# Kernel optimization log

Measured on AMD Instinct MI355X. Metric: run time of the kernel, lower is better.

## Reference

```python
import jax, jax.numpy as jnp
import numpy as np
import math

HIDDEN = 1024
HEADS = 16

def setup_inputs() -> dict:
    key = jax.random.key(0)
    k1, k2, k3 = jax.random.split(key, 3)
    B, T, C = 4, 2048, HIDDEN
    x = jax.random.normal(k1, (B, T, C), dtype=jnp.float32)
    w_qkv = jax.random.normal(k2, (C, 3 * C), dtype=jnp.float32) * (1.0 / math.sqrt(C))
    b_qkv = jnp.zeros((3 * C,), dtype=jnp.float32)
    w_out = jax.random.normal(k3, (C, C), dtype=jnp.float32) * (1.0 / math.sqrt(C))
    b_out = jnp.zeros((C,), dtype=jnp.float32)
    return {"x": x, "w_qkv": w_qkv, "b_qkv": b_qkv, "w_out": w_out, "b_out": b_out}

def reference(x, w_qkv, b_qkv, w_out, b_out):
    B, T, C = x.shape
    H = HEADS
    D = C // H  # head dim
    qkv = x @ w_qkv + b_qkv  # [B,T,3C]
    q, k, v = jnp.split(qkv, 3, axis=2)
    # [B,T,C] -> [B,H,T,D]
    q = q.reshape(B, T, H, D).transpose(0, 2, 1, 3)
    k = k.reshape(B, T, H, D).transpose(0, 2, 1, 3)
    v = v.reshape(B, T, H, D).transpose(0, 2, 1, 3)
    scale = 1.0 / math.sqrt(D)
    logits = jnp.einsum('bhqd,bhkd->bhqk', q, k) * scale  # [B,H,T,T]
    causal = jnp.tril(jnp.ones((T, T), dtype=bool))
    logits = jnp.where(causal[None, None, :, :], logits, -jnp.inf)
    probs = jax.nn.softmax(logits, axis=-1)
    out = jnp.einsum('bhqk,bhkd->bhqd', probs, v)  # [B,H,T,D]
    out = out.transpose(0, 2, 1, 3).reshape(B, T, C)
    return out @ w_out + b_out
```

## Files before the change

### kernel.cpp

```cpp
#include <hip/hip_runtime.h>
#include <hip/hip_bf16.h>

#define C_DIM  1024
#define NHEAD  16
#define DHEAD  64
#define T_LEN  2048
#define B_SZ   4
#define M_ROWS (B_SZ * T_LEN)
#define QKV_N  (3 * C_DIM)

typedef __bf16 bf16x8 __attribute__((ext_vector_type(8)));
typedef float  f32x4  __attribute__((ext_vector_type(4)));
typedef unsigned short ushort8_t __attribute__((ext_vector_type(8)));
typedef unsigned int   uint4_t   __attribute__((ext_vector_type(4)));
typedef short          short4_t  __attribute__((ext_vector_type(4)));

#if __has_builtin(__builtin_amdgcn_mfma_f32_16x16x16bf16_1k)
#define HAVE_MFMA_X16 1
#else
#define HAVE_MFMA_X16 0
#endif

__device__ __forceinline__ unsigned short f2bf(float f) {
    union { float f; unsigned int u; } v; v.f = f;
    unsigned int r = v.u + 0x7FFFu + ((v.u >> 16) & 1u);
    return (unsigned short)(r >> 16);
}

__device__ __forceinline__ bf16x8 as_bf16x8(ushort8_t u) {
    return __builtin_bit_cast(bf16x8, u);
}

__device__ __forceinline__ f32x4 mfma16(bf16x8 a, bf16x8 b, f32x4 c) {
    return __builtin_amdgcn_mfma_f32_16x16x32_bf16(a, b, c, 0, 0, 0);
}

#define GLL16(gsrc, ldst) __builtin_amdgcn_global_load_lds( \
    (const __attribute__((address_space(1))) void*)(gsrc),  \
    (__attribute__((address_space(3))) void*)(ldst), 16, 0, 0)

__device__ __forceinline__ int xcd_remap(int id, int nwg) {
    const int q = nwg >> 3, r = nwg & 7;
    const int xcd = id & 7, off = id >> 3;
    return (xcd < r) ? (xcd * (q + 1) + off) : (r * (q + 1) + (xcd - r) * q + off);
}

__global__ void k_convert(const float* __restrict__ in, unsigned short* __restrict__ out, int n4) {
    int i = blockIdx.x * blockDim.x + threadIdx.x;
    if (i >= n4) return;
    const float4 v = ((const float4*)in)[i];
    unsigned int lo = (unsigned int)f2bf(v.x) | ((unsigned int)f2bf(v.y) << 16);
    unsigned int hi = (unsigned int)f2bf(v.z) | ((unsigned int)f2bf(v.w) << 16);
    ((uint2*)out)[i] = make_uint2(lo, hi);
}

__global__ void k_transpose_bf16(const float* __restrict__ w, unsigned short* __restrict__ wT,
                                 int K, int N) {
    __shared__ float tile[32][33];
    const int n0 = blockIdx.x * 32, k0 = blockIdx.y * 32;
    const int tx = threadIdx.x, ty = threadIdx.y;
    for (int i = 0; i < 32; i += 8)
        tile[ty + i][tx] = w[(size_t)(k0 + ty + i) * N + (n0 + tx)];
    __syncthreads();
    for (int i = 0; i < 32; i += 8)
        wT[(size_t)(n0 + ty + i) * K + (k0 + tx)] = f2bf(tile[tx][ty + i]);
}

__global__ void k_transpose_v(const unsigned short* __restrict__ qkv,
                              unsigned short* __restrict__ vtg) {
    __shared__ unsigned short tile[32][33];
    const int tt = blockIdx.x;
    const int dy = blockIdx.y;
    const int bh = dy >> 1, dtile = dy & 1;
    const int b = bh >> 4, h = bh & 15;
    const int t0 = tt * 32, d0 = dtile * 32;
    const int tx = threadIdx.x, ty = threadIdx.y;
    const unsigned short* src = qkv + (size_t)b * T_LEN * QKV_N + 2 * C_DIM + h * DHEAD + d0;
    for (int i = 0; i < 32; i += 8)
        tile[ty + i][tx] = src[(size_t)(t0 + ty + i) * QKV_N + tx];
    __syncthreads();
    unsigned short* dst = vtg + ((size_t)bh * DHEAD + d0) * T_LEN + t0;
    for (int i = 0; i < 32; i += 8)
        dst[(size_t)(ty + i) * T_LEN + tx] = tile[tx][ty + i];
}

template<int BF16_OUT>
__global__ __launch_bounds__(256) void k_gemm(const unsigned short* __restrict__ A,
                       const unsigned short* __restrict__ Bt,
                       const float* __restrict__ bias,
                       void* __restrict__ C,
                       unsigned short* __restrict__ vtg,
                       int M, int N, int K) {
    __shared__ unsigned short As[128][64];
    __shared__ unsigned short Bs[128][64];

    const int tid  = threadIdx.x;
    const int lane = tid & 63;
    const int wv   = tid >> 6;
    const int wm = wv >> 1, wn = wv & 1;

    const int nwg = gridDim.x * gridDim.y;
    const int wg  = xcd_remap(blockIdx.y * gridDim.x + blockIdx.x, nwg);
    const int bx = wg % gridDim.x, by = wg / gridDim.x;
    const int m0 = by * 128;
    const int n0 = bx * 128;
    const int lr = lane & 15, lg = lane >> 4;

    f32x4 acc[4][4];
#pragma unroll
    for (int i = 0; i < 4; i++)
#pragma unroll
        for (int j = 0; j < 4; j++) acc[i][j] = (f32x4){0.f, 0.f, 0.f, 0.f};

    const int gr = lane >> 3;
    const int gc = 8 * ((lane & 7) ^ gr);

    for (int kt = 0; kt < K; kt += 64) {
        __syncthreads();
#pragma unroll
        for (int j = 0; j < 4; j++) {
            const int row = 32 * wv + 8 * j;
            GLL16(A  + (size_t)(m0 + row + gr) * K + kt + gc, &As[row][0]);
            GLL16(Bt + (size_t)(n0 + row + gr) * K + kt + gc, &Bs[row][0]);
        }
        __syncthreads();

#pragma unroll
        for (int s = 0; s < 2; s++) {
            const int cb = (s * 64 + lg * 16) ^ ((lr & 7) << 4);
            bf16x8 af[4], bfr[4];
#pragma unroll
            for (int i = 0; i < 4; i++)
                af[i] = as_bf16x8(*(const ushort8_t*)((const char*)&As[wm * 64 + i * 16 + lr][0] + cb));
#pragma unroll
            for (int j = 0; j < 4; j++)
                bfr[j] = as_bf16x8(*(const ushort8_t*)((const char*)&Bs[wn * 64 + j * 16 + lr][0] + cb));
#pragma unroll
            for (int i = 0; i < 4; i++)
#pragma unroll
                for (int j = 0; j < 4; j++)
                    acc[i][j] = mfma16(af[i], bfr[j], acc[i][j]);
        }
    }

    const bool isV = (vtg != nullptr) && (n0 >= 2 * C_DIM);
#pragma unroll
    for (int i = 0; i < 4; i++) {
#pragma unroll
        for (int j = 0; j < 4; j++) {
            const int col = n0 + wn * 64 + j * 16 + lr;
            const float bv = bias ? bias[col] : 0.f;
            if (isV) {
                const int dcol = col - 2 * C_DIM;
                const int hh = dcol >> 6, dd = dcol & 63;
                const int row0 = m0 + wm * 64 + i * 16 + lg * 4;
                const int bb = row0 >> 11, t0 = row0 & (T_LEN - 1);
                const unsigned int p0 = (unsigned int)f2bf(acc[i][j][0] + bv)
                                      | ((unsigned int)f2bf(acc[i][j][1] + bv) << 16);
                const unsigned int p1 = (unsigned int)f2bf(acc[i][j][2] + bv)
                                      | ((unsigned int)f2bf(acc[i][j][3] + bv) << 16);
                *(uint2*)&vtg[(((size_t)(bb * 16 + hh)) * 64 + dd) * T_LEN + t0] = make_uint2(p0, p1);
            } else {
#pragma unroll
                for (int r = 0; r < 4; r++) {
                    const int row = m0 + wm * 64 + i * 16 + lg * 4 + r;
                    const float v = acc[i][j][r] + bv;
                    if (BF16_OUT)
                        ((unsigned short*)C)[(size_t)row * N + col] = f2bf(v);
                    else
                        ((float*)C)[(size_t)row * N + col] = v;
                }
            }
        }
    }
}

#define KS_OFF(B_, ROW_) (((B_) << 13) + ((ROW_) << 7))
#define VS_OFF(B_, ROW_) (16384 + ((B_) << 13) + ((ROW_) << 7))
#define SCALE2 0.180336880f
__global__ __launch_bounds__(256, 2) void k_attn(const unsigned short* __restrict__ qkv,
                                                 const unsigned short* __restrict__ vtg,
                                                 unsigned short* __restrict__ out) {
    __shared__ __align__(16) char smem[32768];

    const int blk = xcd_remap(blockIdx.x, B_SZ * NHEAD * 16);
    const int pr = blk & 15;
    const int h  = (blk >> 4) & 15;
    const int b  = blk >> 8;
    const int bh = b * 16 + h;

    const int tid  = threadIdx.x;
    const int lane = tid & 63;
    const int w    = tid >> 6;
    const int lr = lane & 15, lg = lane >> 4;
    const int gr = lane >> 3;
    const int gc = 8 * ((lane & 7) ^ gr);
    const int ra = w * 16;

    const size_t base = (size_t)b * T_LEN * QKV_N + (size_t)h * DHEAD;
    const unsigned short* Qp = qkv + base;
    const unsigned short* Kp = qkv + base + C_DIM;
    const unsigned short* Vt = vtg + (size_t)bh * DHEAD * T_LEN;

    int buf = 0;
    for (int t = 0; t < 2; t++) {
        const int qt = (t == 0) ? pr : (31 - pr);
        const int qw = qt * 64 + w * 16;
        const int qg = qw + lr;
        const int R  = qt + 1;

        bf16x8 qf[2];
#pragma unroll
        for (int s = 0; s < 2; s++)
            qf[s] = as_bf16x8(*(const ushort8_t*)&Qp[(size_t)(qw + lr) * QKV_N + s * 32 + lg * 8]);

        f32x4 o[4];
#pragma unroll
        for (int f = 0; f < 4; f++) o[f] = (f32x4){0.f, 0.f, 0.f, 0.f};
        float lp = 0.f;

        GLL16(Kp + (size_t)(ra + gr) * QKV_N + gc,          smem + KS_OFF(buf, ra));
        GLL16(Kp + (size_t)(ra + 8 + gr) * QKV_N + gc,      smem + KS_OFF(buf, ra + 8));
        GLL16(Vt + (size_t)(ra + gr) * T_LEN + gc,          smem + VS_OFF(buf, ra));
        GLL16(Vt + (size_t)(ra + 8 + gr) * T_LEN + gc,      smem + VS_OFF(buf, ra + 8));

        for (int r = 0; r < R; ++r) {
            const int kb = r * 64;

            asm volatile("s_waitcnt vmcnt(0)" ::: "memory");
            __builtin_amdgcn_s_barrier();
            __builtin_amdgcn_sched_barrier(0);

            if (r + 1 < R) {
                const int kn = kb + 64;
                GLL16(Kp + (size_t)(kn + ra + gr) * QKV_N + gc,     smem + KS_OFF(buf ^ 1, ra));
                GLL16(Kp + (size_t)(kn + ra + 8 + gr) * QKV_N + gc, smem + KS_OFF(buf ^ 1, ra + 8));
                GLL16(Vt + (size_t)(ra + gr) * T_LEN + kn + gc,     smem + VS_OFF(buf ^ 1, ra));
                GLL16(Vt + (size_t)(ra + 8 + gr) * T_LEN + kn + gc, smem + VS_OFF(buf ^ 1, ra + 8));
            }

            f32x4 s4[4];
            __builtin_amdgcn_s_setprio(1);
#pragma unroll
            for (int f = 0; f < 4; f++) {
                const int row = f * 16 + lr;
                const bf16x8 kf0 = as_bf16x8(*(const ushort8_t*)
                    (smem + KS_OFF(buf, row) + ((lg * 16) ^ ((lr & 7) << 4))));
                const bf16x8 kf1 = as_bf16x8(*(const ushort8_t*)
                    (smem + KS_OFF(buf, row) + ((64 + lg * 16) ^ ((lr & 7) << 4))));
                f32x4 s = (f32x4){0.f, 0.f, 0.f, 0.f};
                s = mfma16(kf0, qf[0], s);
                s = mfma16(kf1, qf[1], s);
                s4[f] = s;
            }
            __builtin_amdgcn_s_setprio(0);

            const bool last = (r == R - 1);
            unsigned int pb[4][2];
#pragma unroll
            for (int f = 0; f < 4; f++) {
                unsigned short hh[4];
#pragma unroll
                for (int rr = 0; rr < 4; rr++) {
                    float sv = fminf(s4[f][rr] * SCALE2, 72.f);
                    if (last) {
                        const int kg = kb + f * 16 + lg * 4 + rr;
                        if (kg > qg) sv = -1e30f;
                    }
                    const float e = __builtin_amdgcn_exp2f(sv);
                    lp += e;
                    hh[rr] = __builtin_bit_cast(unsigned short, (__bf16)e);
                }
                pb[f][0] = (unsigned int)hh[0] | ((unsigned int)hh[1] << 16);
                pb[f][1] = (unsigned int)hh[2] | ((unsigned int)hh[3] << 16);
            }

            __builtin_amdgcn_s_setprio(1);
#pragma unroll
            for (int kg = 0; kg < 4; kg++) {
#if HAVE_MFMA_X16
                const short4_t pbv = __builtin_bit_cast(short4_t,
                    make_uint2(pb[kg][0], pb[kg][1]));
#else
                uint4_t pw;
                pw.x = pb[kg][0]; pw.y = pb[kg][1]; pw.z = 0u; pw.w = 0u;
                const bf16x8 pbv8 = __builtin_bit_cast(bf16x8, pw);
#endif
#pragma unroll
                for (int fd = 0; fd < 4; fd++) {
                    const int drow = fd * 16 + lr;
                    const uint2 va = *(const uint2*)(smem + VS_OFF(buf, drow) +
                                     ((kg * 32 + lg * 8) ^ ((lr & 7) << 4)));
#if HAVE_MFMA_X16
                    o[fd] = __builtin_amdgcn_mfma_f32_16x16x16bf16_1k(
                        __builtin_bit_cast(short4_t, va), pbv, o[fd], 0, 0, 0);
#else
                    uint4_t vw;
                    vw.x = va.x; vw.y = va.y; vw.z = va.x; vw.w = va.y;
                    o[fd] = mfma16(__builtin_bit_cast(bf16x8, vw), pbv8, o[fd]);
#endif
                }
            }
            __builtin_amdgcn_s_setprio(0);

            buf ^= 1;
        }

        lp += __shfl_xor(lp, 16, 64);
        lp += __shfl_xor(lp, 32, 64);
        const float inv = 1.f / lp;

#pragma unroll
        for (int fd = 0; fd < 4; fd++)
#pragma unroll
            for (int rr = 0; rr < 4; rr++) {
                const int d = fd * 16 + lg * 4 + rr;
                out[((size_t)b * T_LEN + qw + lr) * C_DIM + h * DHEAD + d] =
                    f2bf(o[fd][rr] * inv);
            }
    }
}

extern "C" void kernel_launch(void* const* d_in, const int* in_sizes, int n_in,
                              void* d_out, int out_size, void* d_ws, size_t ws_size,
                              hipStream_t stream) {
    const float* x      = (const float*)d_in[0];
    const float* w_qkv  = (const float*)d_in[1];
    const float* b_qkv  = (const float*)d_in[2];
    const float* w_out  = (const float*)d_in[3];
    const float* b_out  = (const float*)d_in[4];
    float* out = (float*)d_out;

    char* ws = (char*)d_ws;
    unsigned short* xb    = (unsigned short*)(ws);
    unsigned short* wqkvT = (unsigned short*)(ws + 16777216);
    unsigned short* woutT = (unsigned short*)(ws + 16777216 + 6291456);
    unsigned short* qkv   = (unsigned short*)(ws + 25165824);
    unsigned short* attn  = (unsigned short*)(ws + 75497472);

    const size_t VTG_OFF = 92274688ull;
    const bool fused_vt = (ws_size >= VTG_OFF + 16777216ull);
    unsigned short* vtg = fused_vt ? (unsigned short*)(ws + VTG_OFF)
                                   : (unsigned short*)(ws);

    {
        const int n4 = M_ROWS * C_DIM / 4;
        k_convert<<<(n4 + 255) / 256, 256, 0, stream>>>(x, xb, n4);
    }
    k_transpose_bf16<<<dim3(QKV_N / 32, C_DIM / 32), dim3(32, 8), 0, stream>>>(w_qkv, wqkvT, C_DIM, QKV_N);
    k_transpose_bf16<<<dim3(C_DIM / 32, C_DIM / 32), dim3(32, 8), 0, stream>>>(w_out, woutT, C_DIM, C_DIM);
    k_gemm<1><<<dim3(QKV_N / 128, M_ROWS / 128), 256, 0, stream>>>(
        xb, wqkvT, b_qkv, qkv, fused_vt ? vtg : nullptr, M_ROWS, QKV_N, C_DIM);
    if (!fused_vt)
        k_transpose_v<<<dim3(T_LEN / 32, 64 * 2), dim3(32, 8), 0, stream>>>(qkv, vtg);
    k_attn<<<B_SZ * NHEAD * 16, 256, 0, stream>>>(qkv, vtg, attn);
    k_gemm<0><<<dim3(C_DIM / 128, M_ROWS / 128), 256, 0, stream>>>(
        attn, woutT, b_out, out, nullptr, M_ROWS, C_DIM, C_DIM);
}
```

Baseline: 169.5 us.

## Use a 256x256-tile, 512-thread GEMM kernel for the QKV projection

Adds a new GEMM kernel for the QKV projection. It uses 256x256 output tiles, 8 waves and 128 KB of double-buffered dynamic LDS. The global-to-LDS loads for the next K tile are split into halves and interleaved with four MFMA phases separated by barriers. The fused V-transpose epilogue moves into the new kernel, and the old 128x128 kernel keeps only the plain output path for the output projection. Larger tiles raise operand reuse but give only 384 workgroups, so occupancy and wave balance may suffer, and the large LDS request may limit residency.

```diff
diff --git a/kernel.cpp b/kernel.cpp
--- a/kernel.cpp
+++ b/kernel.cpp
@@ -29,6 +29,10 @@
 
 __device__ __forceinline__ bf16x8 as_bf16x8(ushort8_t u) {
     return __builtin_bit_cast(bf16x8, u);
+}
+
+__device__ __forceinline__ bf16x8 ldsb(const char* p) {
+    return as_bf16x8(*(const ushort8_t*)p);
 }
 
 __device__ __forceinline__ f32x4 mfma16(bf16x8 a, bf16x8 b, f32x4 c) {
@@ -84,12 +88,191 @@
         dst[(size_t)(ty + i) * T_LEN + tx] = tile[tx][ty + i];
 }
 
+#define AS2(B_, R_) ((B_) * 32768 + (R_) * 128)
+#define BS2(B_, R_) (65536 + (B_) * 32768 + (R_) * 128)
+template<int BF16_OUT>
+__global__ __launch_bounds__(512, 2) void k_gemm256(const unsigned short* __restrict__ A,
+                       const unsigned short* __restrict__ Bt,
+                       const float* __restrict__ bias,
+                       void* __restrict__ C,
+                       unsigned short* __restrict__ vtg,
+                       int M, int N, int K) {
+    extern __shared__ char smem[];
+
+    const int tid  = threadIdx.x;
+    const int lane = tid & 63;
+    const int wv   = tid >> 6;
+    const int wm = wv >> 2, wn = wv & 3;
+    const int lr = lane & 15, lg = lane >> 4;
+    const int gr8 = lane >> 3;
+    const int gc  = 8 * ((lane & 7) ^ gr8);
+
+    const int gx  = gridDim.x;
+    const int nwg = gx * gridDim.y;
+    const int wg  = xcd_remap(blockIdx.y * gx + blockIdx.x, nwg);
+    const int bx = wg % gx, by = wg / gx;
+    const int m0 = by * 256, n0 = bx * 256;
+
+    f32x4 acc[8][4];
+#pragma unroll
+    for (int mi = 0; mi < 8; mi++)
+#pragma unroll
+        for (int ni = 0; ni < 4; ni++) acc[mi][ni] = (f32x4){0.f, 0.f, 0.f, 0.f};
+
+    {
+        const int R0 = wv * 16, R1 = 128 + wv * 16;
+        GLL16(A  + (size_t)(m0 + R0 + gr8) * K + gc,     smem + AS2(0, R0));
+        GLL16(A  + (size_t)(m0 + R0 + 8 + gr8) * K + gc, smem + AS2(0, R0 + 8));
+        GLL16(Bt + (size_t)(n0 + R0 + gr8) * K + gc,     smem + BS2(0, R0));
+        GLL16(Bt + (size_t)(n0 + R0 + 8 + gr8) * K + gc, smem + BS2(0, R0 + 8));
+        GLL16(A  + (size_t)(m0 + R1 + gr8) * K + gc,     smem + AS2(0, R1));
+        GLL16(A  + (size_t)(m0 + R1 + 8 + gr8) * K + gc, smem + AS2(0, R1 + 8));
+        GLL16(Bt + (size_t)(n0 + R1 + gr8) * K + gc,     smem + BS2(0, R1));
+        GLL16(Bt + (size_t)(n0 + R1 + 8 + gr8) * K + gc, smem + BS2(0, R1 + 8));
+    }
+
+    const int cb0 = (lg * 16) ^ ((lr & 7) << 4);
+    const int cb1 = (64 + lg * 16) ^ ((lr & 7) << 4);
+
+    int buf = 0;
+    for (int kt = 0; kt < K; kt += 64) {
+        const bool hn = (kt + 64 < K);
+        const int ktn = kt + 64;
+        const int bufn = buf ^ 1;
+
+        asm volatile("s_waitcnt vmcnt(0)" ::: "memory");
+        __builtin_amdgcn_s_barrier();
+        __builtin_amdgcn_sched_barrier(0);
+
+        bf16x8 af[4][2], bfv[2][2];
+
+        if (hn) {
+            const int R0 = wv * 16;
+            GLL16(A  + (size_t)(m0 + R0 + gr8) * K + ktn + gc,     smem + AS2(bufn, R0));
+            GLL16(A  + (size_t)(m0 + R0 + 8 + gr8) * K + ktn + gc, smem + AS2(bufn, R0 + 8));
+            GLL16(Bt + (size_t)(n0 + R0 + gr8) * K + ktn + gc,     smem + BS2(bufn, R0));
+            GLL16(Bt + (size_t)(n0 + R0 + 8 + gr8) * K + ktn + gc, smem + BS2(bufn, R0 + 8));
+        }
+#pragma unroll
+        for (int mi = 0; mi < 4; mi++) {
+            const char* p = smem + AS2(buf, wm * 128 + mi * 16 + lr);
+            af[mi][0] = ldsb(p + cb0); af[mi][1] = ldsb(p + cb1);
+        }
+#pragma unroll
+        for (int ni = 0; ni < 2; ni++) {
+            const char* p = smem + BS2(buf, wn * 64 + ni * 16 + lr);
+            bfv[ni][0] = ldsb(p + cb0); bfv[ni][1] = ldsb(p + cb1);
+        }
+        __builtin_amdgcn_s_setprio(1);
+#pragma unroll
+        for (int ks = 0; ks < 2; ks++)
+#pragma unroll
+            for (int mi = 0; mi < 4; mi++)
+#pragma unroll
+                for (int ni = 0; ni < 2; ni++)
+                    acc[mi][ni] = mfma16(af[mi][ks], bfv[ni][ks], acc[mi][ni]);
+        __builtin_amdgcn_s_setprio(0);
+        __builtin_amdgcn_s_barrier();
+
+        if (hn) {
+            const int R1 = 128 + wv * 16;
+            GLL16(A  + (size_t)(m0 + R1 + gr8) * K + ktn + gc,     smem + AS2(bufn, R1));
+            GLL16(A  + (size_t)(m0 + R1 + 8 + gr8) * K + ktn + gc, smem + AS2(bufn, R1 + 8));
+            GLL16(Bt + (size_t)(n0 + R1 + gr8) * K + ktn + gc,     smem + BS2(bufn, R1));
+            GLL16(Bt + (size_t)(n0 + R1 + 8 + gr8) * K + ktn + gc, smem + BS2(bufn, R1 + 8));
+        }
+#pragma unroll
+        for (int ni = 0; ni < 2; ni++) {
+            const char* p = smem + BS2(buf, wn * 64 + (2 + ni) * 16 + lr);
+            bfv[ni][0] = ldsb(p + cb0); bfv[ni][1] = ldsb(p + cb1);
+        }
+        __builtin_amdgcn_s_setprio(1);
+#pragma unroll
+        for (int ks = 0; ks < 2; ks++)
+#pragma unroll
+            for (int mi = 0; mi < 4; mi++)
+#pragma unroll
+                for (int ni = 0; ni < 2; ni++)
+                    acc[mi][2 + ni] = mfma16(af[mi][ks], bfv[ni][ks], acc[mi][2 + ni]);
+        __builtin_amdgcn_s_setprio(0);
+        __builtin_amdgcn_s_barrier();
+
+#pragma unroll
+        for (int mi = 0; mi < 4; mi++) {
+            const char* p = smem + AS2(buf, wm * 128 + (4 + mi) * 16 + lr);
+            af[mi][0] = ldsb(p + cb0); af[mi][1] = ldsb(p + cb1);
+        }
+#pragma unroll
+        for (int ni = 0; ni < 2; ni++) {
+            const char* p = smem + BS2(buf, wn * 64 + ni * 16 + lr);
+            bfv[ni][0] = ldsb(p + cb0); bfv[ni][1] = ldsb(p + cb1);
+        }
+        __builtin_amdgcn_s_setprio(1);
+#pragma unroll
+        for (int ks = 0; ks < 2; ks++)
+#pragma unroll
+            for (int mi = 0; mi < 4; mi++)
+#pragma unroll
+                for (int ni = 0; ni < 2; ni++)
+                    acc[4 + mi][ni] = mfma16(af[mi][ks], bfv[ni][ks], acc[4 + mi][ni]);
+        __builtin_amdgcn_s_setprio(0);
+        __builtin_amdgcn_s_barrier();
+
+#pragma unroll
+        for (int ni = 0; ni < 2; ni++) {
+            const char* p = smem + BS2(buf, wn * 64 + (2 + ni) * 16 + lr);
+            bfv[ni][0] = ldsb(p + cb0); bfv[ni][1] = ldsb(p + cb1);
+        }
+        __builtin_amdgcn_s_setprio(1);
+#pragma unroll
+        for (int ks = 0; ks < 2; ks++)
+#pragma unroll
+            for (int mi = 0; mi < 4; mi++)
+#pragma unroll
+                for (int ni = 0; ni < 2; ni++)
+                    acc[4 + mi][2 + ni] = mfma16(af[mi][ks], bfv[ni][ks], acc[4 + mi][2 + ni]);
+        __builtin_amdgcn_s_setprio(0);
+
+        buf = bufn;
+    }
+
+    const bool isV = (vtg != nullptr) && (n0 >= 2 * C_DIM);
+#pragma unroll
+    for (int mi = 0; mi < 8; mi++) {
+        const int row0 = m0 + wm * 128 + mi * 16 + lg * 4;
+#pragma unroll
+        for (int ni = 0; ni < 4; ni++) {
+            const int col = n0 + wn * 64 + ni * 16 + lr;
+            const float bv = bias ? bias[col] : 0.f;
+            if (isV) {
+                const int dcol = col - 2 * C_DIM;
+                const int hh = dcol >> 6, dd = dcol & 63;
+                const int bb = row0 >> 11, t0 = row0 & (T_LEN - 1);
+                const unsigned int p0 = (unsigned int)f2bf(acc[mi][ni][0] + bv)
+                                      | ((unsigned int)f2bf(acc[mi][ni][1] + bv) << 16);
+                const unsigned int p1 = (unsigned int)f2bf(acc[mi][ni][2] + bv)
+                                      | ((unsigned int)f2bf(acc[mi][ni][3] + bv) << 16);
+                *(uint2*)&vtg[(((size_t)(bb * 16 + hh)) * 64 + dd) * T_LEN + t0] = make_uint2(p0, p1);
+            } else {
+#pragma unroll
+                for (int rr = 0; rr < 4; rr++) {
+                    const int row = row0 + rr;
+                    const float v = acc[mi][ni][rr] + bv;
+                    if (BF16_OUT)
+                        ((unsigned short*)C)[(size_t)row * N + col] = f2bf(v);
+                    else
+                        ((float*)C)[(size_t)row * N + col] = v;
+                }
+            }
+        }
+    }
+}
+
 template<int BF16_OUT>
 __global__ __launch_bounds__(256) void k_gemm(const unsigned short* __restrict__ A,
                        const unsigned short* __restrict__ Bt,
                        const float* __restrict__ bias,
                        void* __restrict__ C,
-                       unsigned short* __restrict__ vtg,
                        int M, int N, int K) {
     __shared__ unsigned short As[128][64];
     __shared__ unsigned short Bs[128][64];
@@ -143,33 +326,20 @@
         }
     }
 
-    const bool isV = (vtg != nullptr) && (n0 >= 2 * C_DIM);
 #pragma unroll
     for (int i = 0; i < 4; i++) {
 #pragma unroll
         for (int j = 0; j < 4; j++) {
             const int col = n0 + wn * 64 + j * 16 + lr;
             const float bv = bias ? bias[col] : 0.f;
-            if (isV) {
-                const int dcol = col - 2 * C_DIM;
-                const int hh = dcol >> 6, dd = dcol & 63;
-                const int row0 = m0 + wm * 64 + i * 16 + lg * 4;
-                const int bb = row0 >> 11, t0 = row0 & (T_LEN - 1);
-                const unsigned int p0 = (unsigned int)f2bf(acc[i][j][0] + bv)
-                                      | ((unsigned int)f2bf(acc[i][j][1] + bv) << 16);
-                const unsigned int p1 = (unsigned int)f2bf(acc[i][j][2] + bv)
-                                      | ((unsigned int)f2bf(acc[i][j][3] + bv) << 16);
-                *(uint2*)&vtg[(((size_t)(bb * 16 + hh)) * 64 + dd) * T_LEN + t0] = make_uint2(p0, p1);
-            } else {
-#pragma unroll
-                for (int r = 0; r < 4; r++) {
-                    const int row = m0 + wm * 64 + i * 16 + lg * 4 + r;
-                    const float v = acc[i][j][r] + bv;
-                    if (BF16_OUT)
-                        ((unsigned short*)C)[(size_t)row * N + col] = f2bf(v);
-                    else
-                        ((float*)C)[(size_t)row * N + col] = v;
-                }
+#pragma unroll
+            for (int r = 0; r < 4; r++) {
+                const int row = m0 + wm * 64 + i * 16 + lg * 4 + r;
+                const float v = acc[i][j][r] + bv;
+                if (BF16_OUT)
+                    ((unsigned short*)C)[(size_t)row * N + col] = f2bf(v);
+                else
+                    ((float*)C)[(size_t)row * N + col] = v;
             }
         }
     }
@@ -181,7 +351,7 @@
 __global__ __launch_bounds__(256, 2) void k_attn(const unsigned short* __restrict__ qkv,
                                                  const unsigned short* __restrict__ vtg,
                                                  unsigned short* __restrict__ out) {
-    __shared__ __align__(16) char smem[32768];
+    __shared__ __align__(16) char asmem[32768];
 
     const int blk = xcd_remap(blockIdx.x, B_SZ * NHEAD * 16);
     const int pr = blk & 15;
@@ -219,10 +389,10 @@
         for (int f = 0; f < 4; f++) o[f] = (f32x4){0.f, 0.f, 0.f, 0.f};
         float lp = 0.f;
 
-        GLL16(Kp + (size_t)(ra + gr) * QKV_N + gc,          smem + KS_OFF(buf, ra));
-        GLL16(Kp + (size_t)(ra + 8 + gr) * QKV_N + gc,      smem + KS_OFF(buf, ra + 8));
-        GLL16(Vt + (size_t)(ra + gr) * T_LEN + gc,          smem + VS_OFF(buf, ra));
-        GLL16(Vt + (size_t)(ra + 8 + gr) * T_LEN + gc,      smem + VS_OFF(buf, ra + 8));
+        GLL16(Kp + (size_t)(ra + gr) * QKV_N + gc,          asmem + KS_OFF(buf, ra));
+        GLL16(Kp + (size_t)(ra + 8 + gr) * QKV_N + gc,      asmem + KS_OFF(buf, ra + 8));
+        GLL16(Vt + (size_t)(ra + gr) * T_LEN + gc,          asmem + VS_OFF(buf, ra));
+        GLL16(Vt + (size_t)(ra + 8 + gr) * T_LEN + gc,      asmem + VS_OFF(buf, ra + 8));
 
         for (int r = 0; r < R; ++r) {
             const int kb = r * 64;
@@ -233,10 +403,10 @@
 
             if (r + 1 < R) {
                 const int kn = kb + 64;
-                GLL16(Kp + (size_t)(kn + ra + gr) * QKV_N + gc,     smem + KS_OFF(buf ^ 1, ra));
-                GLL16(Kp + (size_t)(kn + ra + 8 + gr) * QKV_N + gc, smem + KS_OFF(buf ^ 1, ra + 8));
-                GLL16(Vt + (size_t)(ra + gr) * T_LEN + kn + gc,     smem + VS_OFF(buf ^ 1, ra));
-                GLL16(Vt + (size_t)(ra + 8 + gr) * T_LEN + kn + gc, smem + VS_OFF(buf ^ 1, ra + 8));
+                GLL16(Kp + (size_t)(kn + ra + gr) * QKV_N + gc,     asmem + KS_OFF(buf ^ 1, ra));
+                GLL16(Kp + (size_t)(kn + ra + 8 + gr) * QKV_N + gc, asmem + KS_OFF(buf ^ 1, ra + 8));
+                GLL16(Vt + (size_t)(ra + gr) * T_LEN + kn + gc,     asmem + VS_OFF(buf ^ 1, ra));
+                GLL16(Vt + (size_t)(ra + 8 + gr) * T_LEN + kn + gc, asmem + VS_OFF(buf ^ 1, ra + 8));
             }
 
             f32x4 s4[4];
@@ -245,9 +415,9 @@
             for (int f = 0; f < 4; f++) {
                 const int row = f * 16 + lr;
                 const bf16x8 kf0 = as_bf16x8(*(const ushort8_t*)
-                    (smem + KS_OFF(buf, row) + ((lg * 16) ^ ((lr & 7) << 4))));
+                    (asmem + KS_OFF(buf, row) + ((lg * 16) ^ ((lr & 7) << 4))));
                 const bf16x8 kf1 = as_bf16x8(*(const ushort8_t*)
-                    (smem + KS_OFF(buf, row) + ((64 + lg * 16) ^ ((lr & 7) << 4))));
+                    (asmem + KS_OFF(buf, row) + ((64 + lg * 16) ^ ((lr & 7) << 4))));
                 f32x4 s = (f32x4){0.f, 0.f, 0.f, 0.f};
                 s = mfma16(kf0, qf[0], s);
                 s = mfma16(kf1, qf[1], s);
@@ -289,7 +459,7 @@
 #pragma unroll
                 for (int fd = 0; fd < 4; fd++) {
                     const int drow = fd * 16 + lr;
-                    const uint2 va = *(const uint2*)(smem + VS_OFF(buf, drow) +
+                    const uint2 va = *(const uint2*)(asmem + VS_OFF(buf, drow) +
                                      ((kg * 32 + lg * 8) ^ ((lr & 7) << 4)));
 #if HAVE_MFMA_X16
                     o[fd] = __builtin_amdgcn_mfma_f32_16x16x16bf16_1k(
@@ -349,11 +519,11 @@
     }
     k_transpose_bf16<<<dim3(QKV_N / 32, C_DIM / 32), dim3(32, 8), 0, stream>>>(w_qkv, wqkvT, C_DIM, QKV_N);
     k_transpose_bf16<<<dim3(C_DIM / 32, C_DIM / 32), dim3(32, 8), 0, stream>>>(w_out, woutT, C_DIM, C_DIM);
-    k_gemm<1><<<dim3(QKV_N / 128, M_ROWS / 128), 256, 0, stream>>>(
+    k_gemm256<1><<<dim3(QKV_N / 256, M_ROWS / 256), 512, 131072, stream>>>(
         xb, wqkvT, b_qkv, qkv, fused_vt ? vtg : nullptr, M_ROWS, QKV_N, C_DIM);
     if (!fused_vt)
         k_transpose_v<<<dim3(T_LEN / 32, 64 * 2), dim3(32, 8), 0, stream>>>(qkv, vtg);
     k_attn<<<B_SZ * NHEAD * 16, 256, 0, stream>>>(qkv, vtg, attn);
     k_gemm<0><<<dim3(C_DIM / 128, M_ROWS / 128), 256, 0, stream>>>(
-        attn, woutT, b_out, out, nullptr, M_ROWS, C_DIM, C_DIM);
-}
+        attn, woutT, b_out, out, M_ROWS, C_DIM, C_DIM);
+}
```

Result: slower. 175.1 us (+3.3%).

## Triple-buffer K/V tiles in attention kernel with two-deep prefetch

Applied to the files above, without the earlier changes.

Changes the K/V shared-memory staging in the attention kernel from double buffering to a three-slot ring, so loads for tile r+2 are issued while tile r is computed. The wait becomes vmcnt(4) instead of vmcnt(0), letting the next tile's loads stay in flight. The aim is to hide more global-load latency. In exchange, LDS per block rises from 32 KB to 48 KB, which may cut the number of resident blocks per CU and hurt occupancy.

```diff
diff --git a/kernel.cpp b/kernel.cpp
--- a/kernel.cpp
+++ b/kernel.cpp
@@ -175,13 +175,13 @@
     }
 }
 
-#define KS_OFF(B_, ROW_) (((B_) << 13) + ((ROW_) << 7))
-#define VS_OFF(B_, ROW_) (16384 + ((B_) << 13) + ((ROW_) << 7))
+#define KS_OFF(B_, ROW_) ((B_) * 16384 + ((ROW_) << 7))
+#define VS_OFF(B_, ROW_) ((B_) * 16384 + 8192 + ((ROW_) << 7))
 #define SCALE2 0.180336880f
 __global__ __launch_bounds__(256, 2) void k_attn(const unsigned short* __restrict__ qkv,
                                                  const unsigned short* __restrict__ vtg,
                                                  unsigned short* __restrict__ out) {
-    __shared__ __align__(16) char smem[32768];
+    __shared__ __align__(16) char asmem[49152];
 
     const int blk = xcd_remap(blockIdx.x, B_SZ * NHEAD * 16);
     const int pr = blk & 15;
@@ -202,7 +202,7 @@
     const unsigned short* Kp = qkv + base + C_DIM;
     const unsigned short* Vt = vtg + (size_t)bh * DHEAD * T_LEN;
 
-    int buf = 0;
+    int cur = 0;
     for (int t = 0; t < 2; t++) {
         const int qt = (t == 0) ? pr : (31 - pr);
         const int qw = qt * 64 + w * 16;
@@ -219,24 +219,36 @@
         for (int f = 0; f < 4; f++) o[f] = (f32x4){0.f, 0.f, 0.f, 0.f};
         float lp = 0.f;
 
-        GLL16(Kp + (size_t)(ra + gr) * QKV_N + gc,          smem + KS_OFF(buf, ra));
-        GLL16(Kp + (size_t)(ra + 8 + gr) * QKV_N + gc,      smem + KS_OFF(buf, ra + 8));
-        GLL16(Vt + (size_t)(ra + gr) * T_LEN + gc,          smem + VS_OFF(buf, ra));
-        GLL16(Vt + (size_t)(ra + 8 + gr) * T_LEN + gc,      smem + VS_OFF(buf, ra + 8));
+        GLL16(Kp + (size_t)(ra + gr) * QKV_N + gc,     asmem + KS_OFF(cur, ra));
+        GLL16(Kp + (size_t)(ra + 8 + gr) * QKV_N + gc, asmem + KS_OFF(cur, ra + 8));
+        GLL16(Vt + (size_t)(ra + gr) * T_LEN + gc,     asmem + VS_OFF(cur, ra));
+        GLL16(Vt + (size_t)(ra + 8 + gr) * T_LEN + gc, asmem + VS_OFF(cur, ra + 8));
+        if (R > 1) {
+            const int b1 = (cur + 1 == 3) ? 0 : cur + 1;
+            GLL16(Kp + (size_t)(64 + ra + gr) * QKV_N + gc,     asmem + KS_OFF(b1, ra));
+            GLL16(Kp + (size_t)(64 + ra + 8 + gr) * QKV_N + gc, asmem + KS_OFF(b1, ra + 8));
+            GLL16(Vt + (size_t)(ra + gr) * T_LEN + 64 + gc,     asmem + VS_OFF(b1, ra));
+            GLL16(Vt + (size_t)(ra + 8 + gr) * T_LEN + 64 + gc, asmem + VS_OFF(b1, ra + 8));
+        }
 
         for (int r = 0; r < R; ++r) {
             const int kb = r * 64;
 
-            asm volatile("s_waitcnt vmcnt(0)" ::: "memory");
+            if (r + 1 < R) {
+                asm volatile("s_waitcnt vmcnt(4)" ::: "memory");
+            } else {
+                asm volatile("s_waitcnt vmcnt(0)" ::: "memory");
+            }
             __builtin_amdgcn_s_barrier();
             __builtin_amdgcn_sched_barrier(0);
 
-            if (r + 1 < R) {
-                const int kn = kb + 64;
-                GLL16(Kp + (size_t)(kn + ra + gr) * QKV_N + gc,     smem + KS_OFF(buf ^ 1, ra));
-                GLL16(Kp + (size_t)(kn + ra + 8 + gr) * QKV_N + gc, smem + KS_OFF(buf ^ 1, ra + 8));
-                GLL16(Vt + (size_t)(ra + gr) * T_LEN + kn + gc,     smem + VS_OFF(buf ^ 1, ra));
-                GLL16(Vt + (size_t)(ra + 8 + gr) * T_LEN + kn + gc, smem + VS_OFF(buf ^ 1, ra + 8));
+            if (r + 2 < R) {
+                const int b2 = (cur + 2 >= 3) ? cur - 1 : cur + 2;
+                const int kn = kb + 128;
+                GLL16(Kp + (size_t)(kn + ra + gr) * QKV_N + gc,     asmem + KS_OFF(b2, ra));
+                GLL16(Kp + (size_t)(kn + ra + 8 + gr) * QKV_N + gc, asmem + KS_OFF(b2, ra + 8));
+                GLL16(Vt + (size_t)(ra + gr) * T_LEN + kn + gc,     asmem + VS_OFF(b2, ra));
+                GLL16(Vt + (size_t)(ra + 8 + gr) * T_LEN + kn + gc, asmem + VS_OFF(b2, ra + 8));
             }
 
             f32x4 s4[4];
@@ -245,9 +257,9 @@
             for (int f = 0; f < 4; f++) {
                 const int row = f * 16 + lr;
                 const bf16x8 kf0 = as_bf16x8(*(const ushort8_t*)
-                    (smem + KS_OFF(buf, row) + ((lg * 16) ^ ((lr & 7) << 4))));
+                    (asmem + KS_OFF(cur, row) + ((lg * 16) ^ ((lr & 7) << 4))));
                 const bf16x8 kf1 = as_bf16x8(*(const ushort8_t*)
-                    (smem + KS_OFF(buf, row) + ((64 + lg * 16) ^ ((lr & 7) << 4))));
+                    (asmem + KS_OFF(cur, row) + ((64 + lg * 16) ^ ((lr & 7) << 4))));
                 f32x4 s = (f32x4){0.f, 0.f, 0.f, 0.f};
                 s = mfma16(kf0, qf[0], s);
                 s = mfma16(kf1, qf[1], s);
@@ -289,7 +301,7 @@
 #pragma unroll
                 for (int fd = 0; fd < 4; fd++) {
                     const int drow = fd * 16 + lr;
-                    const uint2 va = *(const uint2*)(smem + VS_OFF(buf, drow) +
+                    const uint2 va = *(const uint2*)(asmem + VS_OFF(cur, drow) +
                                      ((kg * 32 + lg * 8) ^ ((lr & 7) << 4)));
 #if HAVE_MFMA_X16
                     o[fd] = __builtin_amdgcn_mfma_f32_16x16x16bf16_1k(
@@ -303,7 +315,7 @@
             }
             __builtin_amdgcn_s_setprio(0);
 
-            buf ^= 1;
+            cur = (cur + 1 == 3) ? 0 : cur + 1;
         }
 
         lp += __shfl_xor(lp, 16, 64);
```

Measured after the change: 177.8 us. 1.05x slower.
